# Optimization experiments

Measured on AMD Instinct MI355X. Metric: run time of the kernel, lower is better.

Reference implementation:

```python
import jax, jax.numpy as jnp
import numpy as np

L, B, D = 2048, 8, 1024
EPS = 1e-5  # torch LayerNorm default


def setup_inputs() -> dict:
    key = jax.random.key(0)
    k1, k2 = jax.random.split(key)
    x = jax.random.normal(k1, (L, B, D), dtype=jnp.float32)
    c = jnp.zeros((B, D), dtype=jnp.float32)
    W_ufr = 0.02 * jax.random.normal(k2, (3 * D, D), dtype=jnp.float32)
    ln_gamma = jnp.ones((D,), dtype=jnp.float32)
    ln_beta = jnp.zeros((D,), dtype=jnp.float32)
    return {"x": x, "c": c, "W_ufr": W_ufr, "ln_gamma": ln_gamma, "ln_beta": ln_beta}


def reference(x, c, W_ufr, ln_gamma, ln_beta):
    # LayerNorm over last dim
    mean = jnp.mean(x, axis=-1, keepdims=True)
    var = jnp.mean(jnp.square(x - mean), axis=-1, keepdims=True)
    x_norm = (x - mean) * jax.lax.rsqrt(var + EPS) * ln_gamma + ln_beta

    # Linear (no bias): [L,B,D] @ [D,3D]
    ufr = jnp.einsum('lbd,ed->lbe', x_norm, W_ufr)
    u, f, r = jnp.split(ufr, 3, axis=-1)
    f_gate = jax.nn.sigmoid(f)
    r_gate = jax.nn.sigmoid(r)

    # Sequential recurrence: c_t = f_t * c_{t-1} + (1 - f_t) * u_t
    def step(c_prev, fu):
        f_t, u_t = fu
        c_t = f_t * c_prev + (1.0 - f_t) * u_t
        return c_t, c_t

    last_c, c_stack = jax.lax.scan(step, c, (f_gate, u))

    hs = r_gate * jnp.tanh(c_stack) + (1.0 - r_gate) * x_norm
    return x + hs, last_c
```

## Files before the change

### kernel.cpp

```cpp
#include <hip/hip_runtime.h>
#include <hip/hip_bf16.h>
#include <stdint.h>

#define L_DIM 2048
#define B_DIM 8
#define D_DIM 1024
#define M_DIM (L_DIM * B_DIM)
#define N_DIM (3 * D_DIM)
#define K_DIM D_DIM
#define CH    (B_DIM * D_DIM)
#define EPSLN 1e-5f
#define NC 32
#define CL (L_DIM / NC)

typedef __attribute__((ext_vector_type(8))) short short8;
typedef __attribute__((ext_vector_type(4))) float floatx4;

static __device__ __forceinline__ float bf16_lo(unsigned int p) {
    union { unsigned int u; float f; } v; v.u = p << 16; return v.f;
}
static __device__ __forceinline__ float bf16_hi(unsigned int p) {
    union { unsigned int u; float f; } v; v.u = p & 0xffff0000u; return v.f;
}
static __device__ __forceinline__ float bf16_to_f32(unsigned short h) {
    union { unsigned int u; float f; } v; v.u = ((unsigned int)h) << 16; return v.f;
}
static __device__ __forceinline__ unsigned short f32_to_bf16(float f) {
    union { float f; unsigned int u; } v;
    v.f = f;
    unsigned int u = v.u;
    u += 0x7fffu + ((u >> 16) & 1u);
    return (unsigned short)(u >> 16);
}
static __device__ __forceinline__ float sigmoidf_fast(float v) {
    return 1.0f / (1.0f + __expf(-v));
}
static __device__ __forceinline__ float tanhf_fast(float c) {
    return 1.0f - 2.0f / (1.0f + __expf(2.0f * c));
}

static __device__ __forceinline__ void async16(const void* g, void* l) {
    __builtin_amdgcn_global_load_lds(
        (const __attribute__((address_space(1))) unsigned int*)g,
        (__attribute__((address_space(3))) unsigned int*)l,
        16, 0, 0);
}

__global__ __launch_bounds__(256) void ln_kernel(const float* __restrict__ x,
                                                 const float* __restrict__ gamma,
                                                 const float* __restrict__ beta,
                                                 unsigned short* __restrict__ xn) {
    const int row = blockIdx.x;
    const int tid = threadIdx.x;
    const float4* xr = (const float4*)(x + (size_t)row * D_DIM);
    float4 v = xr[tid];
    float s  = v.x + v.y + v.z + v.w;
    float s2 = v.x * v.x + v.y * v.y + v.z * v.z + v.w * v.w;
    #pragma unroll
    for (int o = 32; o > 0; o >>= 1) {
        s  += __shfl_xor(s, o, 64);
        s2 += __shfl_xor(s2, o, 64);
    }
    __shared__ float red[8];
    const int wid = tid >> 6;
    if ((tid & 63) == 0) { red[wid] = s; red[4 + wid] = s2; }
    __syncthreads();
    s  = red[0] + red[1] + red[2] + red[3];
    s2 = red[4] + red[5] + red[6] + red[7];
    const float mean = s * (1.0f / D_DIM);
    const float var  = s2 * (1.0f / D_DIM) - mean * mean;
    const float rstd = rsqrtf(var + EPSLN);
    const int col = tid * 4;
    const float4 g = *(const float4*)(gamma + col);
    const float4 b = *(const float4*)(beta + col);
    unsigned short o0 = f32_to_bf16((v.x - mean) * rstd * g.x + b.x);
    unsigned short o1 = f32_to_bf16((v.y - mean) * rstd * g.y + b.y);
    unsigned short o2 = f32_to_bf16((v.z - mean) * rstd * g.z + b.z);
    unsigned short o3 = f32_to_bf16((v.w - mean) * rstd * g.w + b.w);
    uint2 packed;
    packed.x = (unsigned int)o0 | ((unsigned int)o1 << 16);
    packed.y = (unsigned int)o2 | ((unsigned int)o3 << 16);
    *(uint2*)(xn + (size_t)row * D_DIM + col) = packed;
}

__global__ __launch_bounds__(256) void wconv_kernel(const float* __restrict__ W,
                                                    unsigned short* __restrict__ Wb) {
    const size_t i = ((size_t)blockIdx.x * 256 + threadIdx.x) * 4;
    float4 v = *(const float4*)(W + i);
    uint2 packed;
    packed.x = (unsigned int)f32_to_bf16(v.x) | ((unsigned int)f32_to_bf16(v.y) << 16);
    packed.y = (unsigned int)f32_to_bf16(v.z) | ((unsigned int)f32_to_bf16(v.w) << 16);
    *(uint2*)(Wb + i) = packed;
}

__global__ __launch_bounds__(256) void gemm_kernel(const unsigned short* __restrict__ A,
                                                   const unsigned short* __restrict__ W,
                                                   unsigned short* __restrict__ u,
                                                   unsigned short* __restrict__ f,
                                                   unsigned short* __restrict__ r) {
    __shared__ __align__(16) unsigned short ldsA[128 * 32];
    __shared__ __align__(16) unsigned short ldsB[128 * 32];
    const int tid  = threadIdx.x;
    const int m0   = blockIdx.y * 128;
    const int n0   = blockIdx.x * 128;
    const int wave = tid >> 6;
    const int lane = tid & 63;
    const int quad = lane >> 4;
    const int l16  = lane & 15;
    const int wm   = (wave >> 1) * 64;
    const int wn   = (wave & 1) * 64;

    floatx4 acc[4][4] = {};

    const int rowS = tid >> 2;
    const int kgS  = (tid & 3) * 8;

    const unsigned short* gA = A + (size_t)(m0 + rowS) * K_DIM + kgS;
    const unsigned short* gB = W + (size_t)(n0 + rowS) * K_DIM + kgS;

    for (int k0 = 0; k0 < K_DIM; k0 += 32) {
        async16(gA + k0,                      &ldsA[(size_t)tid * 8]);
        async16(gA + k0 + (size_t)64 * K_DIM, &ldsA[(size_t)(256 + tid) * 8]);
        async16(gB + k0,                      &ldsB[(size_t)tid * 8]);
        async16(gB + k0 + (size_t)64 * K_DIM, &ldsB[(size_t)(256 + tid) * 8]);
        __syncthreads();

        short8 a[4], b[4];
        #pragma unroll
        for (int i = 0; i < 4; i++) {
            a[i] = *(const short8*)&ldsA[(wm + i * 16 + l16) * 32 + quad * 8];
            b[i] = *(const short8*)&ldsB[(wn + i * 16 + l16) * 32 + quad * 8];
        }
        #pragma unroll
        for (int i = 0; i < 4; i++)
            #pragma unroll
            for (int j = 0; j < 4; j++)
                acc[i][j] = __builtin_amdgcn_mfma_f32_16x16x32_bf16(a[i], b[j], acc[i][j], 0, 0, 0);
        __syncthreads();
    }

    const int region = n0 >> 10;
    const int nn0 = (n0 & 1023) + wn;
    unsigned short* dst = (region == 0) ? u : ((region == 1) ? f : r);
    const bool sig = (region != 0);
    #pragma unroll
    for (int i = 0; i < 4; i++) {
        #pragma unroll
        for (int j = 0; j < 4; j++) {
            #pragma unroll
            for (int t = 0; t < 4; t++) {
                const int gm = m0 + wm + i * 16 + quad * 4 + t;
                const int nn = nn0 + j * 16 + l16;
                float v = acc[i][j][t];
                if (sig) v = sigmoidf_fast(v);
                dst[(size_t)gm * D_DIM + nn] = f32_to_bf16(v);
            }
        }
    }
}

__global__ __launch_bounds__(256) void scan_reduce(const unsigned short* __restrict__ f,
                                                   const unsigned short* __restrict__ u,
                                                   float* __restrict__ Ac,
                                                   float* __restrict__ bc) {
    const int ch2   = (blockIdx.x * 256 + threadIdx.x) * 2;
    const int chunk = blockIdx.y;
    const size_t base = (size_t)chunk * CL * CH + ch2;
    float A0 = 1.0f, b0 = 0.0f, A1 = 1.0f, b1 = 0.0f;
    #pragma unroll 8
    for (int i = 0; i < CL; i++) {
        const size_t idx = base + (size_t)i * CH;
        const unsigned int fp = *(const unsigned int*)(f + idx);
        const unsigned int up = *(const unsigned int*)(u + idx);
        const float f0 = bf16_lo(fp), f1 = bf16_hi(fp);
        const float u0 = bf16_lo(up), u1 = bf16_hi(up);
        b0 = f0 * (b0 - u0) + u0;
        b1 = f1 * (b1 - u1) + u1;
        A0 *= f0;
        A1 *= f1;
    }
    *(float2*)(Ac + chunk * CH + ch2) = make_float2(A0, A1);
    *(float2*)(bc + chunk * CH + ch2) = make_float2(b0, b1);
}

__global__ __launch_bounds__(256) void scan_spine(const float* __restrict__ Ac,
                                                  const float* __restrict__ bc,
                                                  const float* __restrict__ c0,
                                                  float* __restrict__ cst) {
    const int ch = blockIdx.x * 256 + threadIdx.x;
    float c = c0[ch];
    #pragma unroll
    for (int j = 0; j < NC; j++) {
        cst[j * CH + ch] = c;
        c = Ac[j * CH + ch] * c + bc[j * CH + ch];
    }
}

__global__ __launch_bounds__(256) void scan_apply(const unsigned short* __restrict__ f,
                                                  const unsigned short* __restrict__ u,
                                                  const unsigned short* __restrict__ r,
                                                  const float* __restrict__ x,
                                                  const unsigned short* __restrict__ xn,
                                                  const float* __restrict__ cst,
                                                  float* __restrict__ out,
                                                  float* __restrict__ lastc) {
    const int ch2   = (blockIdx.x * 256 + threadIdx.x) * 2;
    const int chunk = blockIdx.y;
    const size_t base = (size_t)chunk * CL * CH + ch2;
    float2 cc = *(const float2*)(cst + chunk * CH + ch2);
    float c0v = cc.x, c1v = cc.y;
    #pragma unroll 4
    for (int i = 0; i < CL; i++) {
        const size_t idx = base + (size_t)i * CH;
        const unsigned int fp = *(const unsigned int*)(f + idx);
        const unsigned int up = *(const unsigned int*)(u + idx);
        const unsigned int rp = *(const unsigned int*)(r + idx);
        const unsigned int xp = *(const unsigned int*)(xn + idx);
        const float2 xv = *(const float2*)(x + idx);
        const float f0 = bf16_lo(fp), f1 = bf16_hi(fp);
        const float u0 = bf16_lo(up), u1 = bf16_hi(up);
        c0v = f0 * (c0v - u0) + u0;
        c1v = f1 * (c1v - u1) + u1;
        const float r0 = bf16_lo(rp), r1 = bf16_hi(rp);
        const float n0 = bf16_lo(xp), n1 = bf16_hi(xp);
        float2 o;
        o.x = xv.x + r0 * tanhf_fast(c0v) + (1.0f - r0) * n0;
        o.y = xv.y + r1 * tanhf_fast(c1v) + (1.0f - r1) * n1;
        *(float2*)(out + idx) = o;
    }
    if (chunk == NC - 1) *(float2*)(lastc + ch2) = make_float2(c0v, c1v);
}

extern "C" void kernel_launch(void* const* d_in, const int* in_sizes, int n_in,
                              void* d_out, int out_size, void* d_ws, size_t ws_size,
                              hipStream_t stream) {
    const float* x     = (const float*)d_in[0];
    const float* c0    = (const float*)d_in[1];
    const float* W     = (const float*)d_in[2];
    const float* gamma = (const float*)d_in[3];
    const float* beta  = (const float*)d_in[4];

    float* out   = (float*)d_out;
    float* lastc = out + (size_t)M_DIM * D_DIM;

    char* ws = (char*)d_ws;
    unsigned short* xn = (unsigned short*)ws;  ws += (size_t)M_DIM * K_DIM * 2;
    unsigned short* Wb = (unsigned short*)ws;  ws += (size_t)N_DIM * K_DIM * 2;
    unsigned short* u  = (unsigned short*)ws;  ws += (size_t)M_DIM * D_DIM * 2;
    unsigned short* f  = (unsigned short*)ws;  ws += (size_t)M_DIM * D_DIM * 2;
    unsigned short* r  = (unsigned short*)ws;  ws += (size_t)M_DIM * D_DIM * 2;
    float* Ac  = (float*)ws;                   ws += (size_t)NC * CH * 4;
    float* bc  = (float*)ws;                   ws += (size_t)NC * CH * 4;
    float* cst = (float*)ws;                   ws += (size_t)NC * CH * 4;

    ln_kernel<<<M_DIM, 256, 0, stream>>>(x, gamma, beta, xn);
    wconv_kernel<<<(N_DIM * K_DIM) / 1024, 256, 0, stream>>>(W, Wb);
    gemm_kernel<<<dim3(N_DIM / 128, M_DIM / 128), 256, 0, stream>>>(xn, Wb, u, f, r);
    scan_reduce<<<dim3(CH / 512, NC), 256, 0, stream>>>(f, u, Ac, bc);
    scan_spine<<<CH / 256, 256, 0, stream>>>(Ac, bc, c0, cst);
    scan_apply<<<dim3(CH / 512, NC), 256, 0, stream>>>(f, u, r, x, xn, cst, out, lastc);
}
```

Baseline: 355.4 us.

## Swizzle GEMM LDS layout, recompute LN in apply, raise scan chunk count

The GEMM's LDS tiles now use an XOR swizzle on the k-chunk index, applied to both the async global-to-LDS writes and the fragment reads, to reduce LDS bank conflicts. The LayerNorm kernel also stores per-row mean and rstd, and scan_apply recomputes x_norm in fp32 from x, which it already loads, so it no longer reads the bf16 xn buffer. This removes a 32 MB read and makes the residual term more precise. The scan chunk count goes from 32 to 128 to give the reduce and apply kernels more parallelism, at the cost of a longer serial spine loop and larger Ac/bc/cst buffers.

```diff
diff --git a/kernel.cpp b/kernel.cpp
--- a/kernel.cpp
+++ b/kernel.cpp
@@ -10,7 +10,7 @@
 #define K_DIM D_DIM
 #define CH    (B_DIM * D_DIM)
 #define EPSLN 1e-5f
-#define NC 32
+#define NC 128
 #define CL (L_DIM / NC)
 
 typedef __attribute__((ext_vector_type(8))) short short8;
@@ -21,9 +21,6 @@
 }
 static __device__ __forceinline__ float bf16_hi(unsigned int p) {
     union { unsigned int u; float f; } v; v.u = p & 0xffff0000u; return v.f;
-}
-static __device__ __forceinline__ float bf16_to_f32(unsigned short h) {
-    union { unsigned int u; float f; } v; v.u = ((unsigned int)h) << 16; return v.f;
 }
 static __device__ __forceinline__ unsigned short f32_to_bf16(float f) {
     union { float f; unsigned int u; } v;
@@ -49,7 +46,9 @@
 __global__ __launch_bounds__(256) void ln_kernel(const float* __restrict__ x,
                                                  const float* __restrict__ gamma,
                                                  const float* __restrict__ beta,
-                                                 unsigned short* __restrict__ xn) {
+                                                 unsigned short* __restrict__ xn,
+                                                 float* __restrict__ meanOut,
+                                                 float* __restrict__ rstdOut) {
     const int row = blockIdx.x;
     const int tid = threadIdx.x;
     const float4* xr = (const float4*)(x + (size_t)row * D_DIM);
@@ -70,6 +69,7 @@
     const float mean = s * (1.0f / D_DIM);
     const float var  = s2 * (1.0f / D_DIM) - mean * mean;
     const float rstd = rsqrtf(var + EPSLN);
+    if (tid == 0) { meanOut[row] = mean; rstdOut[row] = rstd; }
     const int col = tid * 4;
     const float4 g = *(const float4*)(gamma + col);
     const float4 b = *(const float4*)(beta + col);
@@ -112,11 +112,14 @@
 
     floatx4 acc[4][4] = {};
 
-    const int rowS = tid >> 2;
-    const int kgS  = (tid & 3) * 8;
+    const int rowS   = tid >> 2;
+    const int chunkS = (tid & 3) ^ ((rowS >> 1) & 3);
+    const int kgS    = chunkS * 8;
 
     const unsigned short* gA = A + (size_t)(m0 + rowS) * K_DIM + kgS;
     const unsigned short* gB = W + (size_t)(n0 + rowS) * K_DIM + kgS;
+
+    const int ksw = (quad ^ ((l16 >> 1) & 3)) * 8;
 
     for (int k0 = 0; k0 < K_DIM; k0 += 32) {
         async16(gA + k0,                      &ldsA[(size_t)tid * 8]);
@@ -128,8 +131,8 @@
         short8 a[4], b[4];
         #pragma unroll
         for (int i = 0; i < 4; i++) {
-            a[i] = *(const short8*)&ldsA[(wm + i * 16 + l16) * 32 + quad * 8];
-            b[i] = *(const short8*)&ldsB[(wn + i * 16 + l16) * 32 + quad * 8];
+            a[i] = *(const short8*)&ldsA[(wm + i * 16 + l16) * 32 + ksw];
+            b[i] = *(const short8*)&ldsB[(wn + i * 16 + l16) * 32 + ksw];
         }
         #pragma unroll
         for (int i = 0; i < 4; i++)
@@ -189,7 +192,7 @@
                                                   float* __restrict__ cst) {
     const int ch = blockIdx.x * 256 + threadIdx.x;
     float c = c0[ch];
-    #pragma unroll
+    #pragma unroll 4
     for (int j = 0; j < NC; j++) {
         cst[j * CH + ch] = c;
         c = Ac[j * CH + ch] * c + bc[j * CH + ch];
@@ -200,29 +203,39 @@
                                                   const unsigned short* __restrict__ u,
                                                   const unsigned short* __restrict__ r,
                                                   const float* __restrict__ x,
-                                                  const unsigned short* __restrict__ xn,
+                                                  const float* __restrict__ meanIn,
+                                                  const float* __restrict__ rstdIn,
+                                                  const float* __restrict__ gamma,
+                                                  const float* __restrict__ beta,
                                                   const float* __restrict__ cst,
                                                   float* __restrict__ out,
                                                   float* __restrict__ lastc) {
     const int ch2   = (blockIdx.x * 256 + threadIdx.x) * 2;
     const int chunk = blockIdx.y;
+    const int bidx  = ch2 >> 10;
+    const int d     = ch2 & 1023;
+    const float2 g  = *(const float2*)(gamma + d);
+    const float2 be = *(const float2*)(beta + d);
     const size_t base = (size_t)chunk * CL * CH + ch2;
     float2 cc = *(const float2*)(cst + chunk * CH + ch2);
     float c0v = cc.x, c1v = cc.y;
     #pragma unroll 4
     for (int i = 0; i < CL; i++) {
+        const int rowLB = (chunk * CL + i) * B_DIM + bidx;
+        const float mu = meanIn[rowLB];
+        const float rs = rstdIn[rowLB];
         const size_t idx = base + (size_t)i * CH;
         const unsigned int fp = *(const unsigned int*)(f + idx);
         const unsigned int up = *(const unsigned int*)(u + idx);
         const unsigned int rp = *(const unsigned int*)(r + idx);
-        const unsigned int xp = *(const unsigned int*)(xn + idx);
         const float2 xv = *(const float2*)(x + idx);
         const float f0 = bf16_lo(fp), f1 = bf16_hi(fp);
         const float u0 = bf16_lo(up), u1 = bf16_hi(up);
         c0v = f0 * (c0v - u0) + u0;
         c1v = f1 * (c1v - u1) + u1;
         const float r0 = bf16_lo(rp), r1 = bf16_hi(rp);
-        const float n0 = bf16_lo(xp), n1 = bf16_hi(xp);
+        const float n0 = (xv.x - mu) * rs * g.x + be.x;
+        const float n1 = (xv.y - mu) * rs * g.y + be.y;
         float2 o;
         o.x = xv.x + r0 * tanhf_fast(c0v) + (1.0f - r0) * n0;
         o.y = xv.y + r1 * tanhf_fast(c1v) + (1.0f - r1) * n1;
@@ -249,14 +262,17 @@
     unsigned short* u  = (unsigned short*)ws;  ws += (size_t)M_DIM * D_DIM * 2;
     unsigned short* f  = (unsigned short*)ws;  ws += (size_t)M_DIM * D_DIM * 2;
     unsigned short* r  = (unsigned short*)ws;  ws += (size_t)M_DIM * D_DIM * 2;
+    float* meanBuf = (float*)ws;               ws += (size_t)M_DIM * 4;
+    float* rstdBuf = (float*)ws;               ws += (size_t)M_DIM * 4;
     float* Ac  = (float*)ws;                   ws += (size_t)NC * CH * 4;
     float* bc  = (float*)ws;                   ws += (size_t)NC * CH * 4;
     float* cst = (float*)ws;                   ws += (size_t)NC * CH * 4;
 
-    ln_kernel<<<M_DIM, 256, 0, stream>>>(x, gamma, beta, xn);
+    ln_kernel<<<M_DIM, 256, 0, stream>>>(x, gamma, beta, xn, meanBuf, rstdBuf);
     wconv_kernel<<<(N_DIM * K_DIM) / 1024, 256, 0, stream>>>(W, Wb);
     gemm_kernel<<<dim3(N_DIM / 128, M_DIM / 128), 256, 0, stream>>>(xn, Wb, u, f, r);
     scan_reduce<<<dim3(CH / 512, NC), 256, 0, stream>>>(f, u, Ac, bc);
     scan_spine<<<CH / 256, 256, 0, stream>>>(Ac, bc, c0, cst);
-    scan_apply<<<dim3(CH / 512, NC), 256, 0, stream>>>(f, u, r, x, xn, cst, out, lastc);
-}
+    scan_apply<<<dim3(CH / 512, NC), 256, 0, stream>>>(f, u, r, x, meanBuf, rstdBuf,
+                                                       gamma, beta, cst, out, lastc);
+}
```

New measurement: 360.1 us. Within noise of the previous version (+1.3%).
